# Kernel tuning notes

Hardware: AMD Instinct MI355X
Metric: run time of the kernel (lower is better)

## Reference

```python
import jax, jax.numpy as jnp
import numpy as np

N_NODES = 100000
N_EDGES = 1600000
D_IN = 128
HID = 128
N_GRAPHS = 500
NODES_PER_GRAPH = N_NODES // N_GRAPHS


def setup_inputs() -> dict:
    key = jax.random.key(0)
    k1, k2, k3, k4 = jax.random.split(key, 4)
    x = jax.random.normal(k1, (N_NODES, D_IN), dtype=jnp.float32)
    edge_index = jax.random.randint(k2, (2, N_EDGES), 0, N_NODES, dtype=jnp.int64)
    scope = jnp.full((N_GRAPHS,), NODES_PER_GRAPH, dtype=jnp.int64)  # sums to N_NODES
    W1 = jax.random.normal(k3, (D_IN, HID), dtype=jnp.float32) * 0.05
    b1 = jnp.zeros((HID,), dtype=jnp.float32)
    W2 = jax.random.normal(k4, (HID, HID), dtype=jnp.float32) * 0.05
    b2 = jnp.zeros((HID,), dtype=jnp.float32)
    return {"x": x, "edge_index": edge_index, "scope": scope,
            "W1": W1, "b1": b1, "W2": W2, "b2": b2}


def gcn_conv(x, src, dst, W, b, n_nodes):
    # PyG GCNConv: add self loops, symmetric normalization D^-1/2 (A+I) D^-1/2,
    # then linear transform and scatter-add aggregation at target nodes.
    h = x @ W  # [N, H]
    loop = jnp.arange(n_nodes, dtype=src.dtype)
    s = jnp.concatenate([src, loop])
    d = jnp.concatenate([dst, loop])
    ones = jnp.ones(s.shape[0], dtype=h.dtype)
    deg = jax.ops.segment_sum(ones, d, num_segments=n_nodes)  # >=1 due to self loops
    dinv = jax.lax.rsqrt(deg)
    norm = dinv[s] * dinv[d]  # [E+N]
    msgs = h[s] * norm[:, None]  # gather + scale, memory bound
    out = jax.ops.segment_sum(msgs, d, num_segments=n_nodes)  # scatter-add
    return out + b


def reference(x, edge_index, scope, W1, b1, W2, b2):
    src, dst = edge_index[0], edge_index[1]
    h = gcn_conv(x, src, dst, W1, b1, N_NODES)
    # NOTE: original calls self.bn1(h) but discards the result; dropout is
    # identity in eval mode, so only ReLU applies between the two convs.
    h = jax.nn.relu(h)
    h2 = gcn_conv(h, src, dst, W2, b2, N_NODES)
    # ragged per-graph mean pooling (torch.split + mean + stack)
    seg = jnp.repeat(jnp.arange(N_GRAPHS), scope, total_repeat_length=N_NODES)
    sums = jax.ops.segment_sum(h2, seg, num_segments=N_GRAPHS)  # [G, H]
    return sums / scope[:, None].astype(h2.dtype)
```

## Files before the change

kernel.cpp:

```cpp
#include <hip/hip_runtime.h>
#include <hip/hip_bf16.h>
#include <stdint.h>

#define NN 100000
#define NE 1600000
#define HD 128
#define NG 500
#define NPG 200

#define NBK 782
#define NBLK 128
#define CHUNK 12500

typedef __attribute__((ext_vector_type(8))) short short8v;
typedef __attribute__((ext_vector_type(4))) float float4v;
typedef __attribute__((ext_vector_type(2))) float float2v;

__device__ __forceinline__ unsigned int packbf(float a, float b) {
  unsigned int ua = __float_as_uint(a), ub = __float_as_uint(b);
  ua += 0x7fffu + ((ua >> 16) & 1u);
  ub += 0x7fffu + ((ub >> 16) & 1u);
  return (ua >> 16) | (ub & 0xffff0000u);
}

__device__ __forceinline__ int edge32(const void* p, int is64, int idx) {
  const int* q = (const int*)p;
  return is64 ? q[2 * idx] : q[idx];
}

__device__ __forceinline__ int detect_is64(const void* edges, int tid, int* sf) {
  if (tid == 0) *sf = 0;
  __syncthreads();
  const unsigned int* p = (const unsigned int*)edges;
  unsigned int e = p[2 * tid], o = p[2 * tid + 1];
  unsigned int m = (e ? 1u : 0u) | (o ? 2u : 0u);
  if (m) atomicOr(sf, (int)m);
  __syncthreads();
  int v = *sf;
  return ((v & 2) == 0) && (v & 1);
}

__global__ __launch_bounds__(256) void k_hist1(const void* __restrict__ edges,
                                               int* __restrict__ hist) {
  __shared__ int lh[1024];
  __shared__ int sf;
  int tid = threadIdx.x, blk = blockIdx.x;
  int f = detect_is64(edges, tid, &sf);
  for (int i = tid; i < NBK; i += 256) lh[i] = 0;
  __syncthreads();
  int e0 = blk * CHUNK, e1 = e0 + CHUNK;
  if (e1 > NE) e1 = NE;
  for (int e = e0 + tid; e < e1; e += 256) {
    int d = edge32(edges, f, NE + e);
    atomicAdd(&lh[d >> 7], 1);
  }
  __syncthreads();
  for (int i = tid; i < NBK; i += 256) hist[i * NBLK + blk] = lh[i];
}

__global__ void k_scan_block(const int* __restrict__ in, int* __restrict__ outv,
                             int* __restrict__ bsums, int n) {
  __shared__ int s[256];
  int tid = threadIdx.x;
  int i = blockIdx.x * 256 + tid;
  int v = (i < n) ? in[i] : 0;
  s[tid] = v;
  __syncthreads();
  for (int off = 1; off < 256; off <<= 1) {
    int t = (tid >= off) ? s[tid - off] : 0;
    __syncthreads();
    s[tid] += t;
    __syncthreads();
  }
  if (i < n) outv[i] = s[tid] - v;
  if (tid == 255) bsums[blockIdx.x] = s[255];
}

__global__ void k_scan_sums(int* __restrict__ bsums, int nb) {
  __shared__ int s[512];
  int tid = threadIdx.x;
  int v = (tid < nb) ? bsums[tid] : 0;
  s[tid] = v;
  __syncthreads();
  for (int off = 1; off < 512; off <<= 1) {
    int t = (tid >= off) ? s[tid - off] : 0;
    __syncthreads();
    s[tid] += t;
    __syncthreads();
  }
  if (tid < nb) bsums[tid] = s[tid] - v;
}

__global__ __launch_bounds__(256) void k_scatter(const void* __restrict__ edges,
                                                 const int* __restrict__ histS,
                                                 const int* __restrict__ bsums,
                                                 unsigned int* __restrict__ sorted) {
  __shared__ int base[1024];
  __shared__ int sf;
  int tid = threadIdx.x, blk = blockIdx.x;
  int f = detect_is64(edges, tid, &sf);
  for (int i = tid; i < NBK; i += 256) {
    int idx = i * NBLK + blk;
    base[i] = histS[idx] + bsums[idx >> 8];
  }
  __syncthreads();
  int e0 = blk * CHUNK, e1 = e0 + CHUNK;
  if (e1 > NE) e1 = NE;
  for (int e = e0 + tid; e < e1; e += 256) {
    int s = edge32(edges, f, e);
    int d = edge32(edges, f, NE + e);
    int pos = atomicAdd(&base[d >> 7], 1);
    sorted[pos] = ((unsigned)(d & 127) << 17) | (unsigned)s;
  }
}

__global__ __launch_bounds__(256) void k_passB2(const unsigned int* __restrict__ sorted,
                                                const int* __restrict__ histS,
                                                const int* __restrict__ bsums,
                                                int* __restrict__ rowstart,
                                                float* __restrict__ dinv,
                                                int* __restrict__ csr) {
  __shared__ int cnt[128];
  __shared__ int sc[256];
  __shared__ int fill[128];
  __shared__ int stage[4096];
  int b = blockIdx.x, tid = threadIdx.x;
  int i0 = b * NBLK;
  int ebase = histS[i0] + bsums[i0 >> 8];
  int eend = NE;
  if (b + 1 < NBK) {
    int i1 = (b + 1) * NBLK;
    eend = histS[i1] + bsums[i1 >> 8];
  }
  int ne = eend - ebase;
  if (tid < 128) { cnt[tid] = 0; fill[tid] = 0; }
  __syncthreads();
  for (int i = tid; i < ne; i += 256) {
    unsigned int r = sorted[ebase + i];
    atomicAdd(&cnt[r >> 17], 1);
  }
  __syncthreads();
  int v = (tid < 128) ? cnt[tid] : 0;
  sc[tid] = v;
  __syncthreads();
  for (int off = 1; off < 256; off <<= 1) {
    int t = (tid >= off) ? sc[tid - off] : 0;
    __syncthreads();
    sc[tid] += t;
    __syncthreads();
  }
  int node = (b << 7) + tid;
  if (tid < 128 && node < NN) {
    rowstart[node] = ebase + sc[tid] - cnt[tid];
    dinv[node] = rsqrtf((float)(cnt[tid] + 1));
  }
  if (b == NBK - 1 && tid == 0) rowstart[NN] = NE;
  __syncthreads();
  for (int i = tid; i < ne; i += 256) {
    unsigned int r = sorted[ebase + i];
    int ld = (int)(r >> 17);
    int pos = atomicAdd(&fill[ld], 1);
    stage[sc[ld] - cnt[ld] + pos] = (int)(r & 0x1FFFFu);
  }
  __syncthreads();
  for (int i = tid; i < ne; i += 256) csr[ebase + i] = stage[i];
}

__global__ __launch_bounds__(256) void k_ordercvt(const int* __restrict__ rowstart,
                                                  const float* __restrict__ dinv,
                                                  const float4* __restrict__ x,
                                                  uint2* __restrict__ xs8,
                                                  const float* __restrict__ W1,
                                                  unsigned int* __restrict__ W1t,
                                                  int* __restrict__ order) {
  __shared__ int h[128];
  __shared__ int sc[256];
  __shared__ int fill[128];
  __shared__ int degs[256];
  int g = blockIdx.x, tid = threadIdx.x;
  if (tid < 128) { h[tid] = 0; fill[tid] = 0; }
  __syncthreads();
  if (tid < NPG) {
    int n = g * NPG + tid;
    int d = rowstart[n + 1] - rowstart[n];
    if (d > 127) d = 127;
    degs[tid] = d;
    atomicAdd(&h[d], 1);
  }
  __syncthreads();
  int v = (tid < 128) ? h[tid] : 0;
  sc[tid] = v;
  __syncthreads();
  for (int off = 1; off < 256; off <<= 1) {
    int t = (tid >= off) ? sc[tid - off] : 0;
    __syncthreads();
    sc[tid] += t;
    __syncthreads();
  }
  if (tid < NPG) {
    int d = degs[tid];
    int pos = sc[d] - h[d] + atomicAdd(&fill[d], 1);
    order[g * NPG + pos] = g * NPG + tid;
  }
  for (int idx = tid; idx < NPG * 16; idx += 256) {
    int node = g * NPG + (idx >> 4);
    int l = idx & 15;
    float s = dinv[node] * 8.f;
    float4 a = x[(size_t)node * 32 + l * 2];
    float4 b = x[(size_t)node * 32 + l * 2 + 1];
    int w0 = __builtin_amdgcn_cvt_pk_fp8_f32(a.x * s, a.y * s, 0, false);
    w0 = __builtin_amdgcn_cvt_pk_fp8_f32(a.z * s, a.w * s, w0, true);
    int w1 = __builtin_amdgcn_cvt_pk_fp8_f32(b.x * s, b.y * s, 0, false);
    w1 = __builtin_amdgcn_cvt_pk_fp8_f32(b.z * s, b.w * s, w1, true);
    xs8[(size_t)node * 16 + l] = make_uint2((unsigned)w0, (unsigned)w1);
  }
  if (g < 32) {
    int e = g * 256 + tid;
    int c = e >> 6, kp = e & 63;
    float w0 = W1[(size_t)(2 * kp) * 128 + c];
    float w1 = W1[(size_t)(2 * kp + 1) * 128 + c];
    W1t[c * 64 + kp] = packbf(w0, w1);
  }
}

__device__ __forceinline__ void accf8(float* a, uint2 v) {
  float2v f;
  f = __builtin_amdgcn_cvt_pk_f32_fp8((int)v.x, false); a[0] += f.x; a[1] += f.y;
  f = __builtin_amdgcn_cvt_pk_f32_fp8((int)v.x, true);  a[2] += f.x; a[3] += f.y;
  f = __builtin_amdgcn_cvt_pk_f32_fp8((int)v.y, false); a[4] += f.x; a[5] += f.y;
  f = __builtin_amdgcn_cvt_pk_f32_fp8((int)v.y, true);  a[6] += f.x; a[7] += f.y;
}

#define AGG_CORE8(IN, NODE, L, A)                                                \
  float A[8] = {0.f, 0.f, 0.f, 0.f, 0.f, 0.f, 0.f, 0.f};                         \
  accf8(A, IN[(size_t)(NODE)*16 + (L)]);                                         \
  {                                                                              \
    int i = rowstart[NODE], end = rowstart[(NODE) + 1];                          \
    for (; i + 7 < end; i += 8) {                                                \
      int s0 = csr[i], s1 = csr[i + 1], s2 = csr[i + 2], s3 = csr[i + 3];        \
      int s4 = csr[i + 4], s5 = csr[i + 5], s6 = csr[i + 6], s7 = csr[i + 7];    \
      uint2 v0 = IN[(size_t)s0 * 16 + (L)];                                      \
      uint2 v1 = IN[(size_t)s1 * 16 + (L)];                                      \
      uint2 v2 = IN[(size_t)s2 * 16 + (L)];                                      \
      uint2 v3 = IN[(size_t)s3 * 16 + (L)];                                      \
      uint2 v4 = IN[(size_t)s4 * 16 + (L)];                                      \
      uint2 v5 = IN[(size_t)s5 * 16 + (L)];                                      \
      uint2 v6 = IN[(size_t)s6 * 16 + (L)];                                      \
      uint2 v7 = IN[(size_t)s7 * 16 + (L)];                                      \
      accf8(A, v0); accf8(A, v1); accf8(A, v2); accf8(A, v3);                    \
      accf8(A, v4); accf8(A, v5); accf8(A, v6); accf8(A, v7);                    \
    }                                                                            \
    for (; i + 3 < end; i += 4) {                                                \
      int s0 = csr[i], s1 = csr[i + 1], s2 = csr[i + 2], s3 = csr[i + 3];        \
      uint2 v0 = IN[(size_t)s0 * 16 + (L)];                                      \
      uint2 v1 = IN[(size_t)s1 * 16 + (L)];                                      \
      uint2 v2 = IN[(size_t)s2 * 16 + (L)];                                      \
      uint2 v3 = IN[(size_t)s3 * 16 + (L)];                                      \
      accf8(A, v0); accf8(A, v1); accf8(A, v2); accf8(A, v3);                    \
    }                                                                            \
    for (; i < end; ++i) {                                                       \
      uint2 v0 = IN[(size_t)csr[i] * 16 + (L)];                                  \
      accf8(A, v0);                                                              \
    }                                                                            \
  }

__global__ __launch_bounds__(256) void k_agg1g(const uint2* __restrict__ in,
                                               const unsigned int* __restrict__ W1t,
                                               const float* __restrict__ bias,
                                               uint2* __restrict__ out,
                                               const int* __restrict__ rowstart,
                                               const int* __restrict__ csr,
                                               const float* __restrict__ dinv,
                                               const int* __restrict__ order) {
  __shared__ uint4 At[16 * 16];
  __shared__ float Ot[16 * 128];
  __shared__ float sdv[16];
  int tid = threadIdx.x;
  int qw = tid >> 4, l = tid & 15;
  int pos = blockIdx.x * 16 + qw;
  int node = order[pos];
  AGG_CORE8(in, node, l, a)
  float dv = dinv[node];
  if (l == 0) sdv[qw] = dv;
  {
    float ds = dv * 0.125f;
    uint4 o;
    o.x = packbf(a[0] * ds, a[1] * ds); o.y = packbf(a[2] * ds, a[3] * ds);
    o.z = packbf(a[4] * ds, a[5] * ds); o.w = packbf(a[6] * ds, a[7] * ds);
    At[qw * 16 + (l ^ (qw & 7))] = o;
  }
  __syncthreads();

  int w = tid >> 6, lane = tid & 63;
  int m = lane & 15, g = lane >> 4;
  float4v acc[2];
  acc[0] = (float4v)0.f;
  acc[1] = (float4v)0.f;
#pragma unroll
  for (int ks = 0; ks < 4; ++ks) {
    int slot = ks * 4 + g;
    short8v af = *(const short8v*)&At[m * 16 + (slot ^ (m & 7))];
#pragma unroll
    for (int t = 0; t < 2; ++t) {
      int c = (w * 2 + t) * 16 + m;
      short8v bf = *(const short8v*)&W1t[c * 64 + ks * 16 + g * 4];
      acc[t] = __builtin_amdgcn_mfma_f32_16x16x32_bf16(af, bf, acc[t], 0, 0, 0);
    }
  }
#pragma unroll
  for (int t = 0; t < 2; ++t) {
    int c = (w * 2 + t) * 16 + m;
    float bl = bias[c];
#pragma unroll
    for (int j = 0; j < 4; ++j) {
      int r = g * 4 + j;
      float v = fmaxf(acc[t][j] + bl, 0.f) * (sdv[r] * 16.f);
      *(float*)((char*)Ot + r * 512 + ((c * 4) ^ ((r & 7) << 4))) = v;
    }
  }
  __syncthreads();
  {
    int s = (qw & 7) << 4;
    const char* base = (const char*)Ot + qw * 512;
    float4 f0 = *(const float4*)(base + ((l * 32) ^ s));
    float4 f1 = *(const float4*)(base + ((l * 32 + 16) ^ s));
    int w0 = __builtin_amdgcn_cvt_pk_fp8_f32(f0.x, f0.y, 0, false);
    w0 = __builtin_amdgcn_cvt_pk_fp8_f32(f0.z, f0.w, w0, true);
    int w1 = __builtin_amdgcn_cvt_pk_fp8_f32(f1.x, f1.y, 0, false);
    w1 = __builtin_amdgcn_cvt_pk_fp8_f32(f1.z, f1.w, w1, true);
    out[(size_t)node * 16 + l] = make_uint2((unsigned)w0, (unsigned)w1);
  }
}

__global__ __launch_bounds__(256) void k_agg2p(const uint2* __restrict__ in,
                                               float* __restrict__ poolsum,
                                               const int* __restrict__ rowstart,
                                               const int* __restrict__ csr,
                                               const float* __restrict__ dinv,
                                               const int* __restrict__ order) {
  __shared__ float sh[16][128];
  int nl = threadIdx.x >> 4, l = threadIdx.x & 15;
  int pos = blockIdx.x * 16 + nl;
  int node = order[pos];
  AGG_CORE8(in, node, l, a)
  float dv = dinv[node];
#pragma unroll
  for (int j = 0; j < 8; ++j) a[j] *= dv;
  *(float4*)&sh[nl][l * 8] = make_float4(a[0], a[1], a[2], a[3]);
  *(float4*)&sh[nl][l * 8 + 4] = make_float4(a[4], a[5], a[6], a[7]);
  __syncthreads();
  int tid = threadIdx.x;
  if (tid < 128) {
    int n0 = blockIdx.x * 16;
    int gA = n0 / NPG;
    int split = (gA + 1) * NPG - n0;
    if (split > 16) split = 16;
    float sA = 0.f, sB = 0.f;
#pragma unroll
    for (int n = 0; n < 16; ++n) {
      float v = sh[n][tid];
      if (n < split) sA += v; else sB += v;
    }
    atomicAdd(&poolsum[gA * 128 + tid], sA);
    if (split < 16) atomicAdd(&poolsum[(gA + 1) * 128 + tid], sB);
  }
}

__global__ __launch_bounds__(256) void k_gemm2s(const float* __restrict__ A,
                                                const float* __restrict__ W,
                                                const float* __restrict__ bias,
                                                float* __restrict__ out, int M, float ascale) {
  __shared__ float As[8][128];
  int tid = threadIdx.x;
  int row0 = blockIdx.x * 8;
  {
    int r = tid >> 5, c4 = (tid & 31) * 4;
    float4 v = make_float4(0.f, 0.f, 0.f, 0.f);
    if (row0 + r < M) v = *(const float4*)&A[(size_t)(row0 + r) * 128 + c4];
    *(float4*)&As[r][c4] = make_float4(v.x * ascale, v.y * ascale, v.z * ascale, v.w * ascale);
  }
  __syncthreads();
  int r = tid >> 5, c0 = (tid & 31) * 4;
  float acc0 = 0.f, acc1 = 0.f, acc2 = 0.f, acc3 = 0.f;
  for (int k = 0; k < 128; ++k) {
    float a = As[r][k];
    float4 wv = *(const float4*)&W[(size_t)k * 128 + c0];
    acc0 = fmaf(a, wv.x, acc0); acc1 = fmaf(a, wv.y, acc1);
    acc2 = fmaf(a, wv.z, acc2); acc3 = fmaf(a, wv.w, acc3);
  }
  if (row0 + r < M) {
    float4 o;
    o.x = acc0 + bias[c0]; o.y = acc1 + bias[c0 + 1];
    o.z = acc2 + bias[c0 + 2]; o.w = acc3 + bias[c0 + 3];
    *(float4*)&out[(size_t)(row0 + r) * 128 + c0] = o;
  }
}

extern "C" void kernel_launch(void* const* d_in, const int* in_sizes, int n_in,
                              void* d_out, int out_size, void* d_ws, size_t ws_size,
                              hipStream_t stream) {
  const float* x  = (const float*)d_in[0];
  const void* edges = d_in[1];
  const float* W1 = (const float*)d_in[3];
  const float* b1 = (const float*)d_in[4];
  const float* W2 = (const float*)d_in[5];
  const float* b2 = (const float*)d_in[6];
  float* out = (float*)d_out;

  char* ws = (char*)d_ws;
  float* poolsum  = (float*)(ws + 0);
  int*   hist     = (int*)(ws + 256000);
  int*   histS    = (int*)(ws + 656384);
  int*   bsums    = (int*)(ws + 1056768);
  int*   rowstart = (int*)(ws + 1058816);
  float* dinv     = (float*)(ws + 1458832);
  int*   order    = (int*)(ws + 1858832);
  unsigned int* W1t = (unsigned int*)(ws + 2258832);
  unsigned int* sorted = (unsigned int*)(ws + 2291600);
  int*   csr      = (int*)(ws + 8691600);
  void*  xs8      = (void*)(ws + 15091600);
  void*  h1s8     = (void*)(ws + 27891600);

  hipMemsetAsync(poolsum, 0, 256000, stream);

  const int NH = NBK * NBLK;

  k_hist1<<<NBLK, 256, 0, stream>>>(edges, hist);
  k_scan_block<<<(NH + 255) / 256, 256, 0, stream>>>(hist, histS, bsums, NH);
  k_scan_sums<<<1, 512, 0, stream>>>(bsums, (NH + 255) / 256);
  k_scatter<<<NBLK, 256, 0, stream>>>(edges, histS, bsums, sorted);
  k_passB2<<<NBK, 256, 0, stream>>>(sorted, histS, bsums, rowstart, dinv, csr);
  k_ordercvt<<<NG, 256, 0, stream>>>(rowstart, dinv, (const float4*)x, (uint2*)xs8,
                                     W1, W1t, order);

  k_agg1g<<<NN / 16, 256, 0, stream>>>((const uint2*)xs8, W1t, b1, (uint2*)h1s8,
                                       rowstart, csr, dinv, order);
  k_agg2p<<<NN / 16, 256, 0, stream>>>((const uint2*)h1s8, poolsum, rowstart, csr, dinv, order);
  k_gemm2s<<<(NG + 7) / 8, 256, 0, stream>>>(poolsum, W2, b2, out, NG, 1.f / 3200.f);
}
```

Before: 199.4 us.

## Fold block-sum scan and poolsum memset into consumer kernels, unroll gather by 16

Removes the single-block k_scan_sums launch. k_scatter and k_passB2 each redo the 391-entry block-sum scan in shared memory, and the poolsum zeroing moves into k_ordercvt, which drops the memset node. The aggregation gather loop gains a 16-wide unrolled stage so more loads are in flight per thread. The trade is redundant scan work in every block, plus higher register pressure in the aggregation kernels.

```diff
diff --git a/kernel.cpp b/kernel.cpp
--- a/kernel.cpp
+++ b/kernel.cpp
@@ -11,6 +11,7 @@
 #define NBK 782
 #define NBLK 128
 #define CHUNK 12500
+#define NSB 391
 
 typedef __attribute__((ext_vector_type(8))) short short8v;
 typedef __attribute__((ext_vector_type(4))) float float4v;
@@ -38,6 +39,26 @@
   __syncthreads();
   int v = *sf;
   return ((v & 2) == 0) && (v & 1);
+}
+
+__device__ __forceinline__ void scan_bsums(const int* __restrict__ bsums, int* sbs, int tid) {
+  __shared__ int stmp[512];
+  int v0 = (tid < NSB) ? bsums[tid] : 0;
+  int v1 = (tid + 256 < NSB) ? bsums[tid + 256] : 0;
+  stmp[tid] = v0;
+  stmp[tid + 256] = v1;
+  __syncthreads();
+  for (int off = 1; off < 512; off <<= 1) {
+    int t0 = (tid >= off) ? stmp[tid - off] : 0;
+    int t1 = (tid + 256 >= off) ? stmp[tid + 256 - off] : 0;
+    __syncthreads();
+    stmp[tid] += t0;
+    stmp[tid + 256] += t1;
+    __syncthreads();
+  }
+  sbs[tid] = stmp[tid] - v0;
+  sbs[tid + 256] = stmp[tid + 256] - v1;
+  __syncthreads();
 }
 
 __global__ __launch_bounds__(256) void k_hist1(const void* __restrict__ edges,
@@ -76,32 +97,19 @@
   if (tid == 255) bsums[blockIdx.x] = s[255];
 }
 
-__global__ void k_scan_sums(int* __restrict__ bsums, int nb) {
-  __shared__ int s[512];
-  int tid = threadIdx.x;
-  int v = (tid < nb) ? bsums[tid] : 0;
-  s[tid] = v;
-  __syncthreads();
-  for (int off = 1; off < 512; off <<= 1) {
-    int t = (tid >= off) ? s[tid - off] : 0;
-    __syncthreads();
-    s[tid] += t;
-    __syncthreads();
-  }
-  if (tid < nb) bsums[tid] = s[tid] - v;
-}
-
 __global__ __launch_bounds__(256) void k_scatter(const void* __restrict__ edges,
                                                  const int* __restrict__ histS,
                                                  const int* __restrict__ bsums,
                                                  unsigned int* __restrict__ sorted) {
   __shared__ int base[1024];
+  __shared__ int sbs[512];
   __shared__ int sf;
   int tid = threadIdx.x, blk = blockIdx.x;
   int f = detect_is64(edges, tid, &sf);
+  scan_bsums(bsums, sbs, tid);
   for (int i = tid; i < NBK; i += 256) {
     int idx = i * NBLK + blk;
-    base[i] = histS[idx] + bsums[idx >> 8];
+    base[i] = histS[idx] + sbs[idx >> 8];
   }
   __syncthreads();
   int e0 = blk * CHUNK, e1 = e0 + CHUNK;
@@ -120,17 +128,19 @@
                                                 int* __restrict__ rowstart,
                                                 float* __restrict__ dinv,
                                                 int* __restrict__ csr) {
+  __shared__ int sbs[512];
   __shared__ int cnt[128];
   __shared__ int sc[256];
   __shared__ int fill[128];
   __shared__ int stage[4096];
   int b = blockIdx.x, tid = threadIdx.x;
+  scan_bsums(bsums, sbs, tid);
   int i0 = b * NBLK;
-  int ebase = histS[i0] + bsums[i0 >> 8];
+  int ebase = histS[i0] + sbs[i0 >> 8];
   int eend = NE;
   if (b + 1 < NBK) {
     int i1 = (b + 1) * NBLK;
-    eend = histS[i1] + bsums[i1 >> 8];
+    eend = histS[i1] + sbs[i1 >> 8];
   }
   int ne = eend - ebase;
   if (tid < 128) { cnt[tid] = 0; fill[tid] = 0; }
@@ -172,13 +182,14 @@
                                                   uint2* __restrict__ xs8,
                                                   const float* __restrict__ W1,
                                                   unsigned int* __restrict__ W1t,
-                                                  int* __restrict__ order) {
+                                                  int* __restrict__ order,
+                                                  float* __restrict__ poolsum) {
   __shared__ int h[128];
   __shared__ int sc[256];
   __shared__ int fill[128];
   __shared__ int degs[256];
   int g = blockIdx.x, tid = threadIdx.x;
-  if (tid < 128) { h[tid] = 0; fill[tid] = 0; }
+  if (tid < 128) { h[tid] = 0; fill[tid] = 0; poolsum[g * 128 + tid] = 0.f; }
   __syncthreads();
   if (tid < NPG) {
     int n = g * NPG + tid;
@@ -236,6 +247,32 @@
   accf8(A, IN[(size_t)(NODE)*16 + (L)]);                                         \
   {                                                                              \
     int i = rowstart[NODE], end = rowstart[(NODE) + 1];                          \
+    for (; i + 15 < end; i += 16) {                                              \
+      int s0 = csr[i], s1 = csr[i + 1], s2 = csr[i + 2], s3 = csr[i + 3];        \
+      int s4 = csr[i + 4], s5 = csr[i + 5], s6 = csr[i + 6], s7 = csr[i + 7];    \
+      int s8 = csr[i + 8], s9 = csr[i + 9], sA = csr[i + 10], sB = csr[i + 11];  \
+      int sC = csr[i + 12], sD = csr[i + 13], sE = csr[i + 14], sF = csr[i + 15];\
+      uint2 v0 = IN[(size_t)s0 * 16 + (L)];                                      \
+      uint2 v1 = IN[(size_t)s1 * 16 + (L)];                                      \
+      uint2 v2 = IN[(size_t)s2 * 16 + (L)];                                      \
+      uint2 v3 = IN[(size_t)s3 * 16 + (L)];                                      \
+      uint2 v4 = IN[(size_t)s4 * 16 + (L)];                                      \
+      uint2 v5 = IN[(size_t)s5 * 16 + (L)];                                      \
+      uint2 v6 = IN[(size_t)s6 * 16 + (L)];                                      \
+      uint2 v7 = IN[(size_t)s7 * 16 + (L)];                                      \
+      uint2 v8 = IN[(size_t)s8 * 16 + (L)];                                      \
+      uint2 v9 = IN[(size_t)s9 * 16 + (L)];                                      \
+      uint2 vA = IN[(size_t)sA * 16 + (L)];                                      \
+      uint2 vB = IN[(size_t)sB * 16 + (L)];                                      \
+      uint2 vC = IN[(size_t)sC * 16 + (L)];                                      \
+      uint2 vD = IN[(size_t)sD * 16 + (L)];                                      \
+      uint2 vE = IN[(size_t)sE * 16 + (L)];                                      \
+      uint2 vF = IN[(size_t)sF * 16 + (L)];                                      \
+      accf8(A, v0); accf8(A, v1); accf8(A, v2); accf8(A, v3);                    \
+      accf8(A, v4); accf8(A, v5); accf8(A, v6); accf8(A, v7);                    \
+      accf8(A, v8); accf8(A, v9); accf8(A, vA); accf8(A, vB);                    \
+      accf8(A, vC); accf8(A, vD); accf8(A, vE); accf8(A, vF);                    \
+    }                                                                            \
     for (; i + 7 < end; i += 8) {                                                \
       int s0 = csr[i], s1 = csr[i + 1], s2 = csr[i + 2], s3 = csr[i + 3];        \
       int s4 = csr[i + 4], s5 = csr[i + 5], s6 = csr[i + 6], s7 = csr[i + 7];    \
@@ -421,17 +458,14 @@
   void*  xs8      = (void*)(ws + 15091600);
   void*  h1s8     = (void*)(ws + 27891600);
 
-  hipMemsetAsync(poolsum, 0, 256000, stream);
-
   const int NH = NBK * NBLK;
 
   k_hist1<<<NBLK, 256, 0, stream>>>(edges, hist);
-  k_scan_block<<<(NH + 255) / 256, 256, 0, stream>>>(hist, histS, bsums, NH);
-  k_scan_sums<<<1, 512, 0, stream>>>(bsums, (NH + 255) / 256);
+  k_scan_block<<<NSB, 256, 0, stream>>>(hist, histS, bsums, NH);
   k_scatter<<<NBLK, 256, 0, stream>>>(edges, histS, bsums, sorted);
   k_passB2<<<NBK, 256, 0, stream>>>(sorted, histS, bsums, rowstart, dinv, csr);
   k_ordercvt<<<NG, 256, 0, stream>>>(rowstart, dinv, (const float4*)x, (uint2*)xs8,
-                                     W1, W1t, order);
+                                     W1, W1t, order, poolsum);
 
   k_agg1g<<<NN / 16, 256, 0, stream>>>((const uint2*)xs8, W1t, b1, (uint2*)h1s8,
                                        rowstart, csr, dinv, order);
```

After: 197.1 us. Within noise of the previous version (-1.2%).
